# Kernel tuning notes

Measured on AMD Instinct MI355X. Metric: run time of the kernel, lower is better.

The kernel has to match this reference:

```python
import jax, jax.numpy as jnp
import numpy as np
from jax.experimental.ode import odeint

B, T, D = 4096, 48, 32
H, L, HID, E, NH = 256, 128, 256, 8, 48


def _gru_encode(X, mask, w_ih, w_hh, b_ih, b_hh, z0_w, z0_b):
    # Reversed-time GRU over T with mask-gated state updates (torch GRUCell math).
    inp = jnp.concatenate([X, mask], axis=-1)  # [B, T, 2D]
    any_obs = (mask.sum(-1, keepdims=True) > 0).astype(jnp.float32)  # [B, T, 1]

    def step(h, xs):
        x_t, obs_t = xs
        gi = x_t @ w_ih.T + b_ih          # [B, 3H]
        gh = h @ w_hh.T + b_hh            # [B, 3H]
        i_r, i_z, i_n = jnp.split(gi, 3, axis=-1)
        h_r, h_z, h_n = jnp.split(gh, 3, axis=-1)
        r = jax.nn.sigmoid(i_r + h_r)
        zg = jax.nn.sigmoid(i_z + h_z)
        n = jnp.tanh(i_n + r * h_n)
        h_new = (1.0 - zg) * n + zg * h
        h = obs_t * h_new + (1.0 - obs_t) * h
        return h, None

    h0 = jnp.zeros((X.shape[0], H), dtype=jnp.float32)
    xs = (jnp.swapaxes(inp, 0, 1), jnp.swapaxes(any_obs, 0, 1))  # time-major
    h, _ = jax.lax.scan(step, h0, xs, reverse=True)  # iterate t = T-1 .. 0
    z0_out = h @ z0_w.T + z0_b
    z0_mean, z0_logvar = jnp.split(z0_out, 2, axis=-1)
    return z0_mean, z0_logvar


def _ode_func(z, t, tproj_w, tproj_b, w1, b1, w2, b2, w3, b3):
    # Sinusoidal time embedding (E=8 -> 4 sin + 4 cos) + small MLP dynamics.
    steps = jnp.arange(1, E // 2 + 1, dtype=jnp.float32)
    pos = t * steps * jnp.pi
    emb = jnp.concatenate([jnp.sin(pos), jnp.cos(pos)])      # [E]
    temb = tproj_w @ emb + tproj_b                            # [E]
    temb = jnp.broadcast_to(temb, (z.shape[0], E))
    h = jnp.tanh(jnp.concatenate([z, temb], axis=-1) @ w1.T + b1)
    h = jnp.tanh(h @ w2.T + b2)
    return h @ w3.T + b3


def _forward(X, mask, gru_w_ih, gru_w_hh, gru_b_ih, gru_b_hh, z0_w, z0_b,
             tproj_w, tproj_b, ode_w1, ode_b1, ode_w2, ode_b2, ode_w3, ode_b3,
             sh_w1, sh_b1, sh_w2, sh_b2):
    z0_mean, z0_logvar = _gru_encode(X, mask, gru_w_ih, gru_w_hh, gru_b_ih, gru_b_hh, z0_w, z0_b)
    z0 = z0_mean  # eval mode: reparameterise returns the mean
    t_pts = jnp.linspace(0.0, 1.0, NH, dtype=jnp.float32)
    # dopri5 adaptive solver, rtol/atol matching the torch module
    z_traj = odeint(_ode_func, z0, t_pts,
                    tproj_w, tproj_b, ode_w1, ode_b1, ode_w2, ode_b2, ode_w3, ode_b3,
                    rtol=1e-3, atol=1e-4)            # [NH, B, L]
    z_traj = jnp.transpose(z_traj, (1, 0, 2))         # [B, NH, L]
    # DeepHit head
    hmid = jax.nn.relu(z_traj @ sh_w1.T + sh_b1)
    hazard = jax.nn.sigmoid((hmid @ sh_w2.T + sh_b2)[..., 0])  # [B, NH]
    log_1mh = jnp.log(1.0 - hazard + 1e-7)
    log_surv = jnp.cumsum(log_1mh, axis=-1)
    log_surv = jnp.concatenate(
        [jnp.zeros((hazard.shape[0], 1), dtype=hazard.dtype), log_surv[:, :-1]], axis=-1)
    survival = jnp.exp(log_surv)
    p_global = 1.0 - survival[:, -1]
    return hazard, survival, z0_mean, z0_logvar, p_global


def setup_inputs() -> dict:
    key = jax.random.key(0)
    ks = jax.random.split(key, 24)
    s = 0.05  # small init scale keeps the ODE dynamics well-conditioned for dopri5
    return {
        "X": jax.random.normal(ks[0], (B, T, D), jnp.float32),
        "mask": jnp.ones((B, T, D), jnp.float32),
        "gru_w_ih": jax.random.normal(ks[1], (3 * H, 2 * D), jnp.float32) * s,
        "gru_w_hh": jax.random.normal(ks[2], (3 * H, H), jnp.float32) * s,
        "gru_b_ih": jax.random.normal(ks[3], (3 * H,), jnp.float32) * s,
        "gru_b_hh": jax.random.normal(ks[4], (3 * H,), jnp.float32) * s,
        "z0_w": jax.random.normal(ks[5], (2 * L, H), jnp.float32) * s,
        "z0_b": jax.random.normal(ks[6], (2 * L,), jnp.float32) * s,
        "tproj_w": jax.random.normal(ks[7], (E, E), jnp.float32) * s,
        "tproj_b": jax.random.normal(ks[8], (E,), jnp.float32) * s,
        "ode_w1": jax.random.normal(ks[9], (HID, L + E), jnp.float32) * s,
        "ode_b1": jax.random.normal(ks[10], (HID,), jnp.float32) * s,
        "ode_w2": jax.random.normal(ks[11], (HID, HID), jnp.float32) * s,
        "ode_b2": jax.random.normal(ks[12], (HID,), jnp.float32) * s,
        "ode_w3": jax.random.normal(ks[13], (L, HID), jnp.float32) * s,
        "ode_b3": jax.random.normal(ks[14], (L,), jnp.float32) * s,
        "sh_w1": jax.random.normal(ks[15], (32, L), jnp.float32) * s,
        "sh_b1": jax.random.normal(ks[16], (32,), jnp.float32) * s,
        "sh_w2": jax.random.normal(ks[17], (1, 32), jnp.float32) * s,
        "sh_b2": jax.random.normal(ks[18], (1,), jnp.float32) * s,
    }


def reference(X, mask, gru_w_ih, gru_w_hh, gru_b_ih, gru_b_hh, z0_w, z0_b,
              tproj_w, tproj_b, ode_w1, ode_b1, ode_w2, ode_b2, ode_w3, ode_b3,
              sh_w1, sh_b1, sh_w2, sh_b2):
    return _forward(X, mask, gru_w_ih, gru_w_hh, gru_b_ih, gru_b_hh, z0_w, z0_b,
                    tproj_w, tproj_b, ode_w1, ode_b1, ode_w2, ode_b2, ode_w3, ode_b3,
                    sh_w1, sh_b1, sh_w2, sh_b2)
```

## Files before the change

### kernel.cpp

```cpp
#include <hip/hip_runtime.h>
#include <math.h>

#define BB 4096
#define TT 48
#define DD 32
#define HH 256
#define LL 128
#define HID 256
#define EE 8
#define NHZ 48
#define NS 8
#define NTEMB (2*NS+1)

typedef __attribute__((ext_vector_type(8))) short bf16x8;
typedef __attribute__((ext_vector_type(4))) float f32x4;

#define MFMA_BF16(a,b,c) __builtin_amdgcn_mfma_f32_16x16x32_bf16((a),(b),(c),0,0,0)

__device__ __forceinline__ float sigm_f(float x) {
    return 1.0f / (1.0f + __expf(-x));
}
__device__ __forceinline__ float tanh_f(float x) {
    x = fminf(fmaxf(x, -15.0f), 15.0f);
    float e = __expf(2.0f * x);
    return (e - 1.0f) / (e + 1.0f);
}
__device__ __forceinline__ float4 axpy4(float s, float4 a, float4 z) {
    return make_float4(fmaf(s, a.x, z.x), fmaf(s, a.y, z.y),
                       fmaf(s, a.z, z.z), fmaf(s, a.w, z.w));
}
__device__ __forceinline__ unsigned short f2bf(float x) {
    union { float f; unsigned u; } a; a.f = x;
    unsigned r = a.u + 0x7FFFu + ((a.u >> 16) & 1u);
    return (unsigned short)(r >> 16);
}


__global__ void temb_k(const float* __restrict__ tproj_w, const float* __restrict__ tproj_b,
                       float* __restrict__ tembs) {
    int i = blockIdx.x * 64 + threadIdx.x;
    if (i >= NTEMB) return;
    float t = (float)i / (float)(2 * NS);
    const float PI = 3.14159265358979323846f;
    float emb[8];
    #pragma unroll
    for (int m = 0; m < 4; ++m) {
        float pos = t * (float)(m + 1) * PI;
        emb[m]     = sinf(pos);
        emb[4 + m] = cosf(pos);
    }
    #pragma unroll
    for (int o = 0; o < 8; ++o) {
        float a = tproj_b[o];
        #pragma unroll
        for (int k = 0; k < 8; ++k) a = fmaf(tproj_w[o * 8 + k], emb[k], a);
        tembs[i * 8 + o] = a;
    }
}

__global__ void tembW1_k(const float* __restrict__ w1, const float* __restrict__ b1,
                         const float* __restrict__ tembs, float* __restrict__ out) {
    int i = blockIdx.x * 256 + threadIdx.x;
    if (i >= NTEMB * 256) return;
    int ti = i >> 8, n = i & 255;
    float a = b1[n];
    #pragma unroll
    for (int k = 0; k < 8; ++k) a = fmaf(w1[n * 136 + 128 + k], tembs[ti * 8 + k], a);
    out[i] = a;
}


__global__ void packBrz_k(const float* __restrict__ w_ih, const float* __restrict__ w_hh,
                          unsigned short* __restrict__ dst) {
    int i = blockIdx.x * 256 + threadIdx.x;
    if (i >= 32 * 10 * 512) return;
    int frag = i >> 9, e = i & 511;
    int lane = e >> 3, j = e & 7;
    int nt = frag / 10, ks = frag % 10;
    int k = ks * 32 + ((lane >> 4) << 3) + j;
    int n = nt * 16 + (lane & 15);
    float v = (k < 64) ? w_ih[n * 64 + k] : w_hh[n * 256 + (k - 64)];
    dst[i] = f2bf(v);
}

__global__ void packB_k(const float* __restrict__ src, unsigned short* __restrict__ dst,
                        int K, int NT, int NKS) {
    int i = blockIdx.x * 256 + threadIdx.x;
    if (i >= NT * NKS * 512) return;
    int frag = i >> 9, e = i & 511;
    int lane = e >> 3, j = e & 7;
    int nt = frag / NKS, ks = frag % NKS;
    int k = ks * 32 + ((lane >> 4) << 3) + j;
    int n = nt * 16 + (lane & 15);
    dst[i] = f2bf(src[n * K + k]);
}


__global__ __launch_bounds__(512, 1) void gru_mfma_k(
    const float* __restrict__ Xp, const float* __restrict__ Mp,
    const unsigned short* __restrict__ Brz,
    const unsigned short* __restrict__ Bnu,
    const unsigned short* __restrict__ Bnh,
    const unsigned short* __restrict__ Bz0,
    const float* __restrict__ b_ih, const float* __restrict__ b_hh,
    const float* __restrict__ z0_b,
    float* __restrict__ out_mean, float* __restrict__ out_lv) {

    __shared__ unsigned short h_bf[16 * 256];
    __shared__ unsigned short u_bf[16 * 64];
    __shared__ unsigned short bnh_lds[16 * 8 * 512];
    __shared__ float obs[16];

    int tid = threadIdx.x, blk = blockIdx.x;
    int lane = tid & 63, w = tid >> 6;
    int l4 = lane >> 4, l15 = lane & 15;

    for (int e = tid; e < 16 * 256; e += 512) h_bf[e] = 0;
    for (int e = tid; e < 8192; e += 512)
        ((f32x4*)bnh_lds)[e] = ((const f32x4*)Bnh)[e];

    float brz0[2], brz1[2], bin_[2], bhn_[2];
    int hcol[2];
    #pragma unroll
    for (int gg = 0; gg < 2; ++gg) {
        int n = (2 * w + gg) * 16 + l15;
        hcol[gg] = n;
        brz0[gg] = b_ih[n]       + b_hh[n];
        brz1[gg] = b_ih[256 + n] + b_hh[256 + n];
        bin_[gg] = b_ih[512 + n];
        bhn_[gg] = b_hh[512 + n];
    }
    float h_st[2][4] = {{0,0,0,0},{0,0,0,0}};

    __syncthreads();

    int arow = l15, asw = (arow & 7) << 4;

    for (int t = TT - 1; t >= 0; --t) {
        if (tid < 256) {
            int r = tid >> 4, c4 = tid & 15;
            const float* base = (c4 < 8 ? Xp : Mp) + (size_t)(blk * 16 + r) * (TT * DD) + t * DD;
            f32x4 v = __builtin_nontemporal_load(((const f32x4*)base) + (c4 & 7));
            ushort4 p;
            p.x = f2bf(v.x); p.y = f2bf(v.y); p.z = f2bf(v.z); p.w = f2bf(v.w);
            int k0 = (c4 < 8) ? c4 * 4 : 32 + (c4 - 8) * 4;
            int off = r * 128 + ((k0 * 2) ^ ((r & 7) << 4));
            *(ushort4*)((char*)u_bf + off) = p;
        }
        if (tid < 16) {
            const f32x4* mrow = (const f32x4*)(Mp + (size_t)(blk * 16 + tid) * (TT * DD) + t * DD);
            float s = 0.0f;
            #pragma unroll
            for (int i = 0; i < 8; ++i) {
                f32x4 v = __builtin_nontemporal_load(mrow + i);
                s += v.x + v.y + v.z + v.w;
            }
            obs[tid] = (s > 0.0f) ? 1.0f : 0.0f;
        }
        bf16x8 ah[8];
        #pragma unroll
        for (int ks = 0; ks < 8; ++ks)
            ah[ks] = *(const bf16x8*)((const char*)h_bf + (arow * 512 + ((ks * 64 + l4 * 16) ^ asw)));
        __syncthreads();

        bf16x8 au[2];
        #pragma unroll
        for (int ks = 0; ks < 2; ++ks)
            au[ks] = *(const bf16x8*)((const char*)u_bf + (arow * 128 + ((ks * 64 + l4 * 16) ^ asw)));

        #pragma unroll
        for (int gg = 0; gg < 2; ++gg) {
            int g = 2 * w + gg;
            f32x4 accr = {0,0,0,0}, accz = {0,0,0,0}, acci = {0,0,0,0}, acch = {0,0,0,0};
            #pragma unroll
            for (int ks = 0; ks < 10; ++ks) {
                bf16x8 a = (ks < 2) ? au[ks] : ah[ks - 2];
                bf16x8 br = *(const bf16x8*)(Brz + ((g * 10 + ks) * 512 + lane * 8));
                bf16x8 bz = *(const bf16x8*)(Brz + (((16 + g) * 10 + ks) * 512 + lane * 8));
                accr = MFMA_BF16(a, br, accr);
                accz = MFMA_BF16(a, bz, accz);
            }
            #pragma unroll
            for (int ks = 0; ks < 2; ++ks) {
                bf16x8 b = *(const bf16x8*)(Bnu + ((g * 2 + ks) * 512 + lane * 8));
                acci = MFMA_BF16(au[ks], b, acci);
            }
            #pragma unroll
            for (int ks = 0; ks < 8; ++ks) {
                bf16x8 b = *(const bf16x8*)(bnh_lds + ((g * 8 + ks) * 512 + lane * 8));
                acch = MFMA_BF16(ah[ks], b, acch);
            }
            #pragma unroll
            for (int q = 0; q < 4; ++q) {
                int m = l4 * 4 + q;
                float rg = sigm_f(accr[q] + brz0[gg]);
                float zg = sigm_f(accz[q] + brz1[gg]);
                float nn = tanh_f(acci[q] + bin_[gg] + rg * (acch[q] + bhn_[gg]));
                float hnew = (1.0f - zg) * nn + zg * h_st[gg][q];
                float o = obs[m];
                float hs = o * hnew + (1.0f - o) * h_st[gg][q];
                h_st[gg][q] = hs;
                int off = m * 512 + ((hcol[gg] * 2) ^ ((m & 7) << 4));
                *(unsigned short*)((char*)h_bf + off) = f2bf(hs);
            }
        }
        __syncthreads();
    }

    bf16x8 ahf[8];
    #pragma unroll
    for (int ks = 0; ks < 8; ++ks)
        ahf[ks] = *(const bf16x8*)((const char*)h_bf + (arow * 512 + ((ks * 64 + l4 * 16) ^ asw)));
    #pragma unroll
    for (int gg = 0; gg < 2; ++gg) {
        int nt = 2 * w + gg;
        f32x4 acc = {0,0,0,0};
        #pragma unroll
        for (int ks = 0; ks < 8; ++ks) {
            bf16x8 b = *(const bf16x8*)(Bz0 + ((nt * 8 + ks) * 512 + lane * 8));
            acc = MFMA_BF16(ahf[ks], b, acc);
        }
        int n = nt * 16 + l15;
        float bb = z0_b[n];
        #pragma unroll
        for (int q = 0; q < 4; ++q) {
            int m = l4 * 4 + q;
            int row = blk * 16 + m;
            float v = acc[q] + bb;
            if (n < 128) out_mean[row * LL + n] = v;
            else         out_lv  [row * LL + (n - 128)] = v;
        }
    }
}


__device__ __forceinline__ void ode_f_mfma(
    const unsigned short* __restrict__ az, unsigned short* __restrict__ h1b,
    unsigned short* __restrict__ h2b, float* __restrict__ fo,
    const unsigned short* __restrict__ B1, const unsigned short* __restrict__ B2,
    const unsigned short* __restrict__ B3,
    const float* __restrict__ tW1,
    float b2n0, float b2n1, float b3n, int lane, int w) {

    int l4 = lane >> 4, l15 = lane & 15;
    int arow = l15, asw = (arow & 7) << 4;

    bf16x8 a4[4];
    #pragma unroll
    for (int ks = 0; ks < 4; ++ks)
        a4[ks] = *(const bf16x8*)((const char*)az + (arow * 256 + ((ks * 64 + l4 * 16) ^ asw)));
    #pragma unroll
    for (int gg = 0; gg < 2; ++gg) {
        int nt = 2 * w + gg, n = nt * 16 + l15;
        f32x4 acc = {0,0,0,0};
        #pragma unroll
        for (int ks = 0; ks < 4; ++ks) {
            bf16x8 b = *(const bf16x8*)(B1 + ((nt * 4 + ks) * 512 + lane * 8));
            acc = MFMA_BF16(a4[ks], b, acc);
        }
        float tb = tW1[n];
        #pragma unroll
        for (int q = 0; q < 4; ++q) {
            int m = l4 * 4 + q;
            float v = tanh_f(acc[q] + tb);
            *(unsigned short*)((char*)h1b + (m * 512 + ((n * 2) ^ ((m & 7) << 4)))) = f2bf(v);
        }
    }
    __syncthreads();

    bf16x8 a8[8];
    #pragma unroll
    for (int ks = 0; ks < 8; ++ks)
        a8[ks] = *(const bf16x8*)((const char*)h1b + (arow * 512 + ((ks * 64 + l4 * 16) ^ asw)));
    #pragma unroll
    for (int gg = 0; gg < 2; ++gg) {
        int nt = 2 * w + gg, n = nt * 16 + l15;
        f32x4 acc = {0,0,0,0};
        #pragma unroll
        for (int ks = 0; ks < 8; ++ks) {
            bf16x8 b = *(const bf16x8*)(B2 + ((nt * 8 + ks) * 512 + lane * 8));
            acc = MFMA_BF16(a8[ks], b, acc);
        }
        float bb = (gg == 0) ? b2n0 : b2n1;
        #pragma unroll
        for (int q = 0; q < 4; ++q) {
            int m = l4 * 4 + q;
            float v = tanh_f(acc[q] + bb);
            *(unsigned short*)((char*)h2b + (m * 512 + ((n * 2) ^ ((m & 7) << 4)))) = f2bf(v);
        }
    }
    __syncthreads();

    #pragma unroll
    for (int ks = 0; ks < 8; ++ks)
        a8[ks] = *(const bf16x8*)((const char*)h2b + (arow * 512 + ((ks * 64 + l4 * 16) ^ asw)));
    {
        f32x4 acc = {0,0,0,0};
        #pragma unroll
        for (int ks = 0; ks < 8; ++ks) {
            bf16x8 b = *(const bf16x8*)(B3 + ((w * 8 + ks) * 512 + lane * 8));
            acc = MFMA_BF16(a8[ks], b, acc);
        }
        int n = w * 16 + l15;
        #pragma unroll
        for (int q = 0; q < 4; ++q)
            fo[(l4 * 4 + q) * 128 + n] = acc[q] + b3n;
    }
    __syncthreads();
}


__global__ __launch_bounds__(512, 2) void ode_head_mfma_k(
    const float* __restrict__ zinit,
    const unsigned short* __restrict__ B1, const unsigned short* __restrict__ B2,
    const unsigned short* __restrict__ B3,
    const float* __restrict__ tembW1, const float* __restrict__ b2, const float* __restrict__ b3,
    const float* __restrict__ shw1g, const float* __restrict__ shb1,
    const float* __restrict__ shw2, const float* __restrict__ shb2,
    float* __restrict__ out_haz, float* __restrict__ out_surv, float* __restrict__ out_pg) {

    __shared__ __align__(16) float bufA [2048];
    __shared__ __align__(16) float bufB [2048];
    __shared__ __align__(16) float bufFP[2048];
    __shared__ __align__(16) float bufFN[2048];
    __shared__ __align__(16) float ztl  [2048];
    __shared__ __align__(16) unsigned short az [16 * 128];
    __shared__ __align__(16) unsigned short h1b[16 * 256];
    __shared__ __align__(16) unsigned short h2b[16 * 256];
    __shared__ __align__(16) float w1h[32 * 128];

    int tid = threadIdx.x, blk = blockIdx.x;
    int lane = tid & 63, w = tid >> 6;
    int l15 = lane & 15;
    int s5 = tid & 31, rh = tid >> 5;

    float b2n0 = b2[(2 * w) * 16 + l15];
    float b2n1 = b2[(2 * w + 1) * 16 + l15];
    float b3n  = b3[w * 16 + l15];
    float w2s = shw2[s5], b1s = shb1[s5], b2s = shb2[0];
    float cum_r = 0.0f;
    const float4* w1hq = (const float4*)w1h;

    float* zA = bufA; float* zB = bufB;
    float* fP = bufFP; float* fN = bufFN;

    int crow = tid >> 5, ccol = (tid & 31) * 4;
    int azoff = crow * 256 + ((ccol * 2) ^ ((crow & 7) << 4));

    {
        float4 zv = ((const float4*)(zinit + (size_t)blk * 2048))[tid];
        ((float4*)zA)[tid] = zv;
        ushort4 pb; pb.x = f2bf(zv.x); pb.y = f2bf(zv.y); pb.z = f2bf(zv.z); pb.w = f2bf(zv.w);
        *(ushort4*)((char*)az + azoff) = pb;
    }
    for (int e = tid; e < 32 * 128; e += 512) {
        int u = e >> 7, k = e & 127;
        w1h[((k >> 2) * 32 + u) * 4 + (k & 3)] = shw1g[e];
    }
    __syncthreads();

    ode_f_mfma(az, h1b, h2b, fP, B1, B2, B3, tembW1, b2n0, b2n1, b3n, lane, w);

    const float Hh = 1.0f / (float)NS;

    for (int st = 0; st < NS; ++st) {
        float4 ka, zr0;
        {
            float4 f = ((const float4*)fP)[tid];
            zr0 = ((const float4*)zA)[tid];
            ka = f;
            float4 zv = axpy4(0.5f * Hh, f, zr0);
            ((float4*)ztl)[tid] = zv;
            ushort4 pb; pb.x=f2bf(zv.x); pb.y=f2bf(zv.y); pb.z=f2bf(zv.z); pb.w=f2bf(zv.w);
            *(ushort4*)((char*)az + azoff) = pb;
        }
        __syncthreads();
        ode_f_mfma(az, h1b, h2b, fN, B1, B2, B3, tembW1 + (2*st+1)*256, b2n0, b2n1, b3n, lane, w);
        {
            float4 f = ((const float4*)fN)[tid];
            ka = axpy4(2.0f, f, ka);
            float4 zv = axpy4(0.5f * Hh, f, zr0);
            ((float4*)ztl)[tid] = zv;
            ushort4 pb; pb.x=f2bf(zv.x); pb.y=f2bf(zv.y); pb.z=f2bf(zv.z); pb.w=f2bf(zv.w);
            *(ushort4*)((char*)az + azoff) = pb;
        }
        __syncthreads();
        ode_f_mfma(az, h1b, h2b, fN, B1, B2, B3, tembW1 + (2*st+1)*256, b2n0, b2n1, b3n, lane, w);
        {
            float4 f = ((const float4*)fN)[tid];
            ka = axpy4(2.0f, f, ka);
            float4 zv = axpy4(Hh, f, zr0);
            ((float4*)ztl)[tid] = zv;
            ushort4 pb; pb.x=f2bf(zv.x); pb.y=f2bf(zv.y); pb.z=f2bf(zv.z); pb.w=f2bf(zv.w);
            *(ushort4*)((char*)az + azoff) = pb;
        }
        __syncthreads();
        ode_f_mfma(az, h1b, h2b, fN, B1, B2, B3, tembW1 + (2*st+2)*256, b2n0, b2n1, b3n, lane, w);
        {
            float4 f = ((const float4*)fN)[tid];
            float s6 = Hh / 6.0f;
            float4 kk = make_float4(ka.x + f.x, ka.y + f.y, ka.z + f.z, ka.w + f.w);
            float4 zv = axpy4(s6, kk, zr0);
            ((float4*)zB)[tid] = zv;
            ushort4 pb; pb.x=f2bf(zv.x); pb.y=f2bf(zv.y); pb.z=f2bf(zv.z); pb.w=f2bf(zv.w);
            *(ushort4*)((char*)az + azoff) = pb;
        }
        __syncthreads();
        ode_f_mfma(az, h1b, h2b, fN, B1, B2, B3, tembW1 + (2*st+2)*256, b2n0, b2n1, b3n, lane, w);

        int jlo = (47 * st + NS - 1) / NS;
        int jhi = (st == NS - 1) ? 47 : (47 * (st + 1) + NS - 1) / NS - 1;
        for (int jp = jlo; jp <= jhi; ++jp) {
            float th  = ((float)NS * (float)jp - 47.0f * (float)st) * (1.0f / 47.0f);
            float th2 = th * th, th3 = th2 * th;
            float c0 = 2.0f * th3 - 3.0f * th2 + 1.0f;
            float c1 = 3.0f * th2 - 2.0f * th3;
            float c2 = Hh * (th3 - 2.0f * th2 + th);
            float c3 = Hh * (th3 - th2);
            {
                float4 za = ((const float4*)zA)[tid];
                float4 zb = ((const float4*)zB)[tid];
                float4 fa = ((const float4*)fP)[tid];
                float4 fb = ((const float4*)fN)[tid];
                float4 zv;
                zv.x = c0*za.x + c1*zb.x + c2*fa.x + c3*fb.x;
                zv.y = c0*za.y + c1*zb.y + c2*fa.y + c3*fb.y;
                zv.z = c0*za.z + c1*zb.z + c2*fa.z + c3*fb.z;
                zv.w = c0*za.w + c1*zb.w + c2*fa.w + c3*fb.w;
                ((float4*)ztl)[tid] = zv;
            }
            __syncthreads();
            {
                float aa = b1s;
                const float4* zrow = (const float4*)(ztl + rh * LL);
                for (int k4 = 0; k4 < 32; ++k4) {
                    float4 wv = w1hq[k4 * 32 + s5];
                    float4 v = zrow[k4];
                    aa = fmaf(wv.x, v.x, aa); aa = fmaf(wv.y, v.y, aa);
                    aa = fmaf(wv.z, v.z, aa); aa = fmaf(wv.w, v.w, aa);
                }
                float p = fmaxf(aa, 0.0f) * w2s;
                p += __shfl_xor(p, 1);  p += __shfl_xor(p, 2);
                p += __shfl_xor(p, 4);  p += __shfl_xor(p, 8);
                p += __shfl_xor(p, 16);
                float hz = sigm_f(p + b2s);
                float sv = __expf(cum_r);
                cum_r += __logf(1.0f - hz + 1e-7f);
                if (s5 == 0) {
                    int row = blk * 16 + rh;
                    out_haz [row * NHZ + jp] = hz;
                    out_surv[row * NHZ + jp] = sv;
                    if (jp == NHZ - 1) out_pg[row] = 1.0f - sv;
                }
            }
            __syncthreads();
        }

        float* t0 = zA; zA = zB; zB = t0;
        t0 = fP; fP = fN; fN = t0;
    }
}


extern "C" void kernel_launch(void* const* d_in, const int* in_sizes, int n_in,
                              void* d_out, int out_size, void* d_ws, size_t ws_size,
                              hipStream_t stream) {
    const float* X        = (const float*)d_in[0];
    const float* Mask     = (const float*)d_in[1];
    const float* gru_w_ih = (const float*)d_in[2];
    const float* gru_w_hh = (const float*)d_in[3];
    const float* gru_b_ih = (const float*)d_in[4];
    const float* gru_b_hh = (const float*)d_in[5];
    const float* z0_w     = (const float*)d_in[6];
    const float* z0_b     = (const float*)d_in[7];
    const float* tproj_w  = (const float*)d_in[8];
    const float* tproj_b  = (const float*)d_in[9];
    const float* ode_w1   = (const float*)d_in[10];
    const float* ode_b1   = (const float*)d_in[11];
    const float* ode_w2   = (const float*)d_in[12];
    const float* ode_b2   = (const float*)d_in[13];
    const float* ode_w3   = (const float*)d_in[14];
    const float* ode_b3   = (const float*)d_in[15];
    const float* sh_w1    = (const float*)d_in[16];
    const float* sh_b1    = (const float*)d_in[17];
    const float* sh_w2    = (const float*)d_in[18];
    const float* sh_b2    = (const float*)d_in[19];

    float* ws     = (float*)d_ws;
    float* tembs  = ws;
    float* tembW1 = ws + 256;
    unsigned short* Brz = (unsigned short*)(ws + 4608);
    unsigned short* Bnu = Brz + 163840;
    unsigned short* Bnh = Bnu + 16384;
    unsigned short* Bz0 = Bnh + 65536;
    unsigned short* B1  = Bz0 + 65536;
    unsigned short* B2  = B1  + 32768;
    unsigned short* B3  = B2  + 65536;

    float* out      = (float*)d_out;
    float* out_haz  = out;
    float* out_surv = out + 196608;
    float* out_mean = out + 393216;
    float* out_lv   = out + 917504;
    float* out_pg   = out + 1441792;

    temb_k<<<1, 64, 0, stream>>>(tproj_w, tproj_b, tembs);
    tembW1_k<<<(NTEMB * 256 + 255) / 256, 256, 0, stream>>>(ode_w1, ode_b1, tembs, tembW1);

    packBrz_k<<<(32*10*512) / 256, 256, 0, stream>>>(gru_w_ih, gru_w_hh, Brz);
    packB_k<<<(16*2*512) / 256, 256, 0, stream>>>(gru_w_ih + 512 * 64,  Bnu, 64,  16, 2);
    packB_k<<<(16*8*512) / 256, 256, 0, stream>>>(gru_w_hh + 512 * 256, Bnh, 256, 16, 8);
    packB_k<<<(16*8*512) / 256, 256, 0, stream>>>(z0_w,                 Bz0, 256, 16, 8);
    packB_k<<<(16*4*512) / 256, 256, 0, stream>>>(ode_w1, B1, 136, 16, 4);
    packB_k<<<(16*8*512) / 256, 256, 0, stream>>>(ode_w2, B2, 256, 16, 8);
    packB_k<<<( 8*8*512) / 256, 256, 0, stream>>>(ode_w3, B3, 256,  8, 8);

    gru_mfma_k<<<BB / 16, 512, 0, stream>>>(X, Mask, Brz, Bnu, Bnh, Bz0,
                                            gru_b_ih, gru_b_hh, z0_b, out_mean, out_lv);

    ode_head_mfma_k<<<BB / 16, 512, 0, stream>>>(out_mean, B1, B2, B3,
                                                 tembW1, ode_b2, ode_b3,
                                                 sh_w1, sh_b1, sh_w2, sh_b2,
                                                 out_haz, out_surv, out_pg);
}
```

Baseline: 440.8 us.

## Process 32 batch rows per GRU block to reuse weight fragments across two M tiles

The GRU encoder block now handles 32 batch rows instead of 16, so each weight fragment loaded from global memory or LDS feeds two MFMA row tiles. This halves weight traffic per row and halves the grid to 128 blocks. The cost is more registers per thread (accumulators, A fragments and state are doubled) and fewer blocks than CUs on MI355X, which may leave compute units idle.

Measured after the change: 757.8 us. +71.9%, slower.

```diff
diff --git a/kernel.cpp b/kernel.cpp
--- a/kernel.cpp
+++ b/kernel.cpp
@@ -11,6 +11,7 @@
 #define NHZ 48
 #define NS 8
 #define NTEMB (2*NS+1)
+#define GROWS 32
 
 typedef __attribute__((ext_vector_type(8))) short bf16x8;
 typedef __attribute__((ext_vector_type(4))) float f32x4;
@@ -106,16 +107,16 @@
     const float* __restrict__ z0_b,
     float* __restrict__ out_mean, float* __restrict__ out_lv) {
 
-    __shared__ unsigned short h_bf[16 * 256];
-    __shared__ unsigned short u_bf[16 * 64];
+    __shared__ unsigned short h_bf[GROWS * 256];
+    __shared__ unsigned short u_bf[GROWS * 64];
     __shared__ unsigned short bnh_lds[16 * 8 * 512];
-    __shared__ float obs[16];
+    __shared__ float obs[GROWS];
 
     int tid = threadIdx.x, blk = blockIdx.x;
     int lane = tid & 63, w = tid >> 6;
     int l4 = lane >> 4, l15 = lane & 15;
 
-    for (int e = tid; e < 16 * 256; e += 512) h_bf[e] = 0;
+    for (int e = tid; e < GROWS * 256; e += 512) h_bf[e] = 0;
     for (int e = tid; e < 8192; e += 512)
         ((f32x4*)bnh_lds)[e] = ((const f32x4*)Bnh)[e];
 
@@ -130,16 +131,20 @@
         bin_[gg] = b_ih[512 + n];
         bhn_[gg] = b_hh[512 + n];
     }
-    float h_st[2][4] = {{0,0,0,0},{0,0,0,0}};
+    float h_st[2][2][4];
+    #pragma unroll
+    for (int gg = 0; gg < 2; ++gg)
+        #pragma unroll
+        for (int mt = 0; mt < 2; ++mt)
+            #pragma unroll
+            for (int q = 0; q < 4; ++q) h_st[gg][mt][q] = 0.0f;
 
     __syncthreads();
 
-    int arow = l15, asw = (arow & 7) << 4;
-
     for (int t = TT - 1; t >= 0; --t) {
-        if (tid < 256) {
+        {
             int r = tid >> 4, c4 = tid & 15;
-            const float* base = (c4 < 8 ? Xp : Mp) + (size_t)(blk * 16 + r) * (TT * DD) + t * DD;
+            const float* base = (c4 < 8 ? Xp : Mp) + (size_t)(blk * GROWS + r) * (TT * DD) + t * DD;
             f32x4 v = __builtin_nontemporal_load(((const f32x4*)base) + (c4 & 7));
             ushort4 p;
             p.x = f2bf(v.x); p.y = f2bf(v.y); p.z = f2bf(v.z); p.w = f2bf(v.w);
@@ -147,8 +152,8 @@
             int off = r * 128 + ((k0 * 2) ^ ((r & 7) << 4));
             *(ushort4*)((char*)u_bf + off) = p;
         }
-        if (tid < 16) {
-            const f32x4* mrow = (const f32x4*)(Mp + (size_t)(blk * 16 + tid) * (TT * DD) + t * DD);
+        if (tid < GROWS) {
+            const f32x4* mrow = (const f32x4*)(Mp + (size_t)(blk * GROWS + tid) * (TT * DD) + t * DD);
             float s = 0.0f;
             #pragma unroll
             for (int i = 0; i < 8; ++i) {
@@ -157,78 +162,102 @@
             }
             obs[tid] = (s > 0.0f) ? 1.0f : 0.0f;
         }
-        bf16x8 ah[8];
-        #pragma unroll
-        for (int ks = 0; ks < 8; ++ks)
-            ah[ks] = *(const bf16x8*)((const char*)h_bf + (arow * 512 + ((ks * 64 + l4 * 16) ^ asw)));
+        bf16x8 ah[2][8];
+        #pragma unroll
+        for (int mt = 0; mt < 2; ++mt) {
+            int arow = mt * 16 + l15, asw = (arow & 7) << 4;
+            #pragma unroll
+            for (int ks = 0; ks < 8; ++ks)
+                ah[mt][ks] = *(const bf16x8*)((const char*)h_bf + (arow * 512 + ((ks * 64 + l4 * 16) ^ asw)));
+        }
         __syncthreads();
 
-        bf16x8 au[2];
-        #pragma unroll
-        for (int ks = 0; ks < 2; ++ks)
-            au[ks] = *(const bf16x8*)((const char*)u_bf + (arow * 128 + ((ks * 64 + l4 * 16) ^ asw)));
+        bf16x8 au[2][2];
+        #pragma unroll
+        for (int mt = 0; mt < 2; ++mt) {
+            int arow = mt * 16 + l15, asw = (arow & 7) << 4;
+            #pragma unroll
+            for (int ks = 0; ks < 2; ++ks)
+                au[mt][ks] = *(const bf16x8*)((const char*)u_bf + (arow * 128 + ((ks * 64 + l4 * 16) ^ asw)));
+        }
 
         #pragma unroll
         for (int gg = 0; gg < 2; ++gg) {
             int g = 2 * w + gg;
-            f32x4 accr = {0,0,0,0}, accz = {0,0,0,0}, acci = {0,0,0,0}, acch = {0,0,0,0};
+            f32x4 accr[2] = {{0,0,0,0},{0,0,0,0}};
+            f32x4 accz[2] = {{0,0,0,0},{0,0,0,0}};
+            f32x4 acci[2] = {{0,0,0,0},{0,0,0,0}};
+            f32x4 acch[2] = {{0,0,0,0},{0,0,0,0}};
             #pragma unroll
             for (int ks = 0; ks < 10; ++ks) {
-                bf16x8 a = (ks < 2) ? au[ks] : ah[ks - 2];
                 bf16x8 br = *(const bf16x8*)(Brz + ((g * 10 + ks) * 512 + lane * 8));
                 bf16x8 bz = *(const bf16x8*)(Brz + (((16 + g) * 10 + ks) * 512 + lane * 8));
-                accr = MFMA_BF16(a, br, accr);
-                accz = MFMA_BF16(a, bz, accz);
+                #pragma unroll
+                for (int mt = 0; mt < 2; ++mt) {
+                    bf16x8 a = (ks < 2) ? au[mt][ks] : ah[mt][ks - 2];
+                    accr[mt] = MFMA_BF16(a, br, accr[mt]);
+                    accz[mt] = MFMA_BF16(a, bz, accz[mt]);
+                }
             }
             #pragma unroll
             for (int ks = 0; ks < 2; ++ks) {
                 bf16x8 b = *(const bf16x8*)(Bnu + ((g * 2 + ks) * 512 + lane * 8));
-                acci = MFMA_BF16(au[ks], b, acci);
+                #pragma unroll
+                for (int mt = 0; mt < 2; ++mt)
+                    acci[mt] = MFMA_BF16(au[mt][ks], b, acci[mt]);
             }
             #pragma unroll
             for (int ks = 0; ks < 8; ++ks) {
                 bf16x8 b = *(const bf16x8*)(bnh_lds + ((g * 8 + ks) * 512 + lane * 8));
-                acch = MFMA_BF16(ah[ks], b, acch);
-            }
+                #pragma unroll
+                for (int mt = 0; mt < 2; ++mt)
+                    acch[mt] = MFMA_BF16(ah[mt][ks], b, acch[mt]);
+            }
+            #pragma unroll
+            for (int mt = 0; mt < 2; ++mt) {
+                #pragma unroll
+                for (int q = 0; q < 4; ++q) {
+                    int m = mt * 16 + l4 * 4 + q;
+                    float rg = sigm_f(accr[mt][q] + brz0[gg]);
+                    float zg = sigm_f(accz[mt][q] + brz1[gg]);
+                    float nn = tanh_f(acci[mt][q] + bin_[gg] + rg * (acch[mt][q] + bhn_[gg]));
+                    float hnew = (1.0f - zg) * nn + zg * h_st[gg][mt][q];
+                    float o = obs[m];
+                    float hs = o * hnew + (1.0f - o) * h_st[gg][mt][q];
+                    h_st[gg][mt][q] = hs;
+                    int off = m * 512 + ((hcol[gg] * 2) ^ ((m & 7) << 4));
+                    *(unsigned short*)((char*)h_bf + off) = f2bf(hs);
+                }
+            }
+        }
+        __syncthreads();
+    }
+
+    #pragma unroll
+    for (int mt = 0; mt < 2; ++mt) {
+        int arow = mt * 16 + l15, asw = (arow & 7) << 4;
+        bf16x8 ahf[8];
+        #pragma unroll
+        for (int ks = 0; ks < 8; ++ks)
+            ahf[ks] = *(const bf16x8*)((const char*)h_bf + (arow * 512 + ((ks * 64 + l4 * 16) ^ asw)));
+        #pragma unroll
+        for (int gg = 0; gg < 2; ++gg) {
+            int nt = 2 * w + gg;
+            f32x4 acc = {0,0,0,0};
+            #pragma unroll
+            for (int ks = 0; ks < 8; ++ks) {
+                bf16x8 b = *(const bf16x8*)(Bz0 + ((nt * 8 + ks) * 512 + lane * 8));
+                acc = MFMA_BF16(ahf[ks], b, acc);
+            }
+            int n = nt * 16 + l15;
+            float bb = z0_b[n];
             #pragma unroll
             for (int q = 0; q < 4; ++q) {
-                int m = l4 * 4 + q;
-                float rg = sigm_f(accr[q] + brz0[gg]);
-                float zg = sigm_f(accz[q] + brz1[gg]);
-                float nn = tanh_f(acci[q] + bin_[gg] + rg * (acch[q] + bhn_[gg]));
-                float hnew = (1.0f - zg) * nn + zg * h_st[gg][q];
-                float o = obs[m];
-                float hs = o * hnew + (1.0f - o) * h_st[gg][q];
-                h_st[gg][q] = hs;
-                int off = m * 512 + ((hcol[gg] * 2) ^ ((m & 7) << 4));
-                *(unsigned short*)((char*)h_bf + off) = f2bf(hs);
-            }
-        }
-        __syncthreads();
-    }
-
-    bf16x8 ahf[8];
-    #pragma unroll
-    for (int ks = 0; ks < 8; ++ks)
-        ahf[ks] = *(const bf16x8*)((const char*)h_bf + (arow * 512 + ((ks * 64 + l4 * 16) ^ asw)));
-    #pragma unroll
-    for (int gg = 0; gg < 2; ++gg) {
-        int nt = 2 * w + gg;
-        f32x4 acc = {0,0,0,0};
-        #pragma unroll
-        for (int ks = 0; ks < 8; ++ks) {
-            bf16x8 b = *(const bf16x8*)(Bz0 + ((nt * 8 + ks) * 512 + lane * 8));
-            acc = MFMA_BF16(ahf[ks], b, acc);
-        }
-        int n = nt * 16 + l15;
-        float bb = z0_b[n];
-        #pragma unroll
-        for (int q = 0; q < 4; ++q) {
-            int m = l4 * 4 + q;
-            int row = blk * 16 + m;
-            float v = acc[q] + bb;
-            if (n < 128) out_mean[row * LL + n] = v;
-            else         out_lv  [row * LL + (n - 128)] = v;
+                int row = blk * GROWS + mt * 16 + l4 * 4 + q;
+                float v = acc[q] + bb;
+                if (n < 128) out_mean[row * LL + n] = v;
+                else         out_lv  [row * LL + (n - 128)] = v;
+            }
         }
     }
 }
@@ -515,8 +544,8 @@
     packB_k<<<(16*8*512) / 256, 256, 0, stream>>>(ode_w2, B2, 256, 16, 8);
     packB_k<<<( 8*8*512) / 256, 256, 0, stream>>>(ode_w3, B3, 256,  8, 8);
 
-    gru_mfma_k<<<BB / 16, 512, 0, stream>>>(X, Mask, Brz, Bnu, Bnh, Bz0,
-                                            gru_b_ih, gru_b_hh, z0_b, out_mean, out_lv);
+    gru_mfma_k<<<BB / GROWS, 512, 0, stream>>>(X, Mask, Brz, Bnu, Bnh, Bz0,
+                                               gru_b_ih, gru_b_hh, z0_b, out_mean, out_lv);
 
     ode_head_mfma_k<<<BB / 16, 512, 0, stream>>>(out_mean, B1, B2, B3,
                                                  tembW1, ode_b2, ode_b3,
```
